# Performance work log

Measured on AMD Instinct MI355X. Metric: run time of the kernel, lower is better.

Reference implementation:

```python
import jax, jax.numpy as jnp
import numpy as np

B, N, K, F_IN, F_OUT = 2, 196608, 9, 64, 64


def setup_inputs() -> dict:
    key = jax.random.key(0)
    k1, k2, k3 = jax.random.split(key, 3)
    x = jax.random.normal(k1, (B, N, F_IN), dtype=jnp.float32)
    adjc = jax.random.randint(k2, (N, K), 0, N, dtype=jnp.int64)
    # first neighbor is the cell itself (typical grid adjacency)
    adjc = adjc.at[:, 0].set(jnp.arange(N, dtype=jnp.int64))
    scale = 1.0 / np.sqrt(K * F_IN)
    W = jax.random.normal(k3, (K, F_IN, F_OUT), dtype=jnp.float32) * scale
    b = jnp.zeros((F_OUT,), dtype=jnp.float32)
    return {"x": x, "adjc": adjc, "W": W, "b": b}


def reference(x, adjc, W, b):
    # get_nh: irregular gather of neighbor features -> [B, N, K, F_in]
    x_nh = x[:, adjc, :]
    # learned layer: contract over (neighborhood, in_features) -> [B, N, F_out]
    out = jnp.einsum("bnkf,kfo->bno", x_nh, W) + b
    return out
```

## Files before the change

### kernel.cpp

```cpp
#include <hip/hip_runtime.h>

#define B_ 2
#define N_ 196608
#define K_ 9
#define F_ 64
#define ROWS 64
#define ROWB 256

typedef __attribute__((ext_vector_type(8))) short short8;
typedef __attribute__((ext_vector_type(4))) unsigned short ushort4v;
typedef __attribute__((ext_vector_type(4))) float f32x4;

__device__ __forceinline__ unsigned short f2bf(float f) {
  unsigned u = __builtin_bit_cast(unsigned, f);
  u = (u + 0x7fffu + ((u >> 16) & 1u)) >> 16;
  return (unsigned short)u;
}

__global__ __launch_bounds__(256) void cvt_x_kernel(const float* __restrict__ x,
                                                    unsigned short* __restrict__ xb) {
  const int b = blockIdx.y;
  const long cidx = (long)blockIdx.x * 256 + threadIdx.x;
  const long n = cidx >> 4;
  const int qd = (int)(cidx & 15);
  const float4 v = *(const float4*)(x + ((size_t)b * N_ + n) * F_ + (size_t)qd * 4);
  ushort4v r;
  r[0] = f2bf(v.x); r[1] = f2bf(v.y); r[2] = f2bf(v.z); r[3] = f2bf(v.w);
  *(ushort4v*)(xb + ((size_t)n * 2 + b) * F_ + qd * 4) = r;
}

__global__ __launch_bounds__(256) void cvt_w_kernel(const float* __restrict__ W,
                                                    unsigned short* __restrict__ wt) {
  const int i = blockIdx.x * 256 + threadIdx.x;
  const int k = i >> 12;
  const int rem = i & 4095;
  const int o = rem >> 6;
  const int f = rem & 63;
  wt[i] = f2bf(W[(k << 12) + (f << 6) + o]);
}

__global__ __launch_bounds__(64, 1) void nhconv_main(
    const short* __restrict__ xb,
    const int* __restrict__ adjc,
    const short* __restrict__ wt,
    const float* __restrict__ bias,
    float* __restrict__ out) {
  __shared__ short abuf[3][ROWS * 128];
  __shared__ int s_adj[ROWS * K_];

  const int l = (int)threadIdx.x;
  const int n0 = blockIdx.x * ROWS;
  const int q = l >> 4;
  const int c = l & 15;

  for (int i = l; i < ROWS * K_; i += 64)
    s_adj[i] = __builtin_nontemporal_load(adjc + (size_t)n0 * K_ + i);

  auto stage = [&](int k, int bf) {
#pragma unroll
    for (int j = 0; j < 16; ++j) {
      const int row = j * 4 + (l >> 4);
      const int src_chunk = (l & 15) ^ (row & 7);
      const size_t goff = (size_t)(unsigned)s_adj[row * K_ + k] * ROWB + (src_chunk << 4);
      const char* src = (const char*)xb + goff;
      short* dst = &abuf[bf][(j * 4) * 128];
      __builtin_amdgcn_global_load_lds(
          (const __attribute__((address_space(1))) unsigned int*)src,
          (__attribute__((address_space(3))) unsigned int*)dst, 16, 0, 0);
    }
  };

  const short* wbase = wt + q * 8 + (c << 6);
  short8 rw[2][8];
  auto wload = [&](int k, int par) {
#pragma unroll
    for (int fs = 0; fs < 2; ++fs)
#pragma unroll
      for (int ct = 0; ct < 4; ++ct)
        rw[par][fs * 4 + ct] = *(const short8*)(wbase + (k << 12) + fs * 32 + (ct << 10));
  };

  f32x4 acc[2][4][4];
#pragma unroll
  for (int p = 0; p < 2; ++p)
#pragma unroll
    for (int rt = 0; rt < 4; ++rt)
#pragma unroll
      for (int ct = 0; ct < 4; ++ct)
        acc[p][rt][ct] = (f32x4){0.f, 0.f, 0.f, 0.f};

  wload(0, 0);
  stage(0, 0);
  wload(1, 1);
  stage(1, 1);

#pragma unroll
  for (int k = 0; k < K_; ++k) {
    asm volatile("s_waitcnt lgkmcnt(0)" ::: "memory");
    if (k >= 1 && k + 1 < K_) wload(k + 1, (k + 1) & 1);
    if (k + 2 < K_) stage(k + 2, (k + 2) % 3);

    if (k <= K_ - 3) {
      asm volatile("s_waitcnt vmcnt(40)" ::: "memory");
    } else if (k == K_ - 2) {
      asm volatile("s_waitcnt vmcnt(24)" ::: "memory");
    } else {
      asm volatile("s_waitcnt vmcnt(0)" ::: "memory");
    }
    __builtin_amdgcn_sched_barrier(0);

    const short* bufk = abuf[k % 3];
#pragma unroll
    for (int fs = 0; fs < 2; ++fs) {
#pragma unroll
      for (int rt = 0; rt < 4; ++rt) {
        const int arow = (rt * 16 + c) * 128;
        const int ch0 = (fs * 4 + q) ^ (c & 7);
        const int ch1 = (8 + fs * 4 + q) ^ (c & 7);
        const short8 a0 = *(const short8*)&bufk[arow + (ch0 << 3)];
        const short8 a1 = *(const short8*)&bufk[arow + (ch1 << 3)];
#pragma unroll
        for (int ct = 0; ct < 4; ++ct) {
          const short8 bfr = rw[k & 1][fs * 4 + ct];
          acc[0][rt][ct] =
              __builtin_amdgcn_mfma_f32_16x16x32_bf16(a0, bfr, acc[0][rt][ct], 0, 0, 0);
          acc[1][rt][ct] =
              __builtin_amdgcn_mfma_f32_16x16x32_bf16(a1, bfr, acc[1][rt][ct], 0, 0, 0);
        }
      }
    }
  }

  float bv[4];
#pragma unroll
  for (int ct = 0; ct < 4; ++ct) bv[ct] = bias[ct * 16 + c];

#pragma unroll
  for (int p = 0; p < 2; ++p) {
    const size_t outbase = ((size_t)p * N_ + (size_t)n0) * F_;
#pragma unroll
    for (int rt = 0; rt < 4; ++rt) {
#pragma unroll
      for (int ct = 0; ct < 4; ++ct) {
#pragma unroll
        for (int rr = 0; rr < 4; ++rr) {
          const int row = rt * 16 + q * 4 + rr;
          __builtin_nontemporal_store(acc[p][rt][ct][rr] + bv[ct],
                                      &out[outbase + (size_t)row * F_ + ct * 16 + c]);
        }
      }
    }
  }
}

extern "C" void kernel_launch(void* const* d_in, const int* in_sizes, int n_in,
                              void* d_out, int out_size, void* d_ws, size_t ws_size,
                              hipStream_t stream) {
  const float* x = (const float*)d_in[0];
  const int* adjc = (const int*)d_in[1];
  const float* W = (const float*)d_in[2];
  const float* bias = (const float*)d_in[3];
  float* out = (float*)d_out;

  unsigned short* xb = (unsigned short*)d_ws;
  unsigned short* wt = (unsigned short*)((char*)d_ws + (size_t)B_ * N_ * F_ * 2);

  cvt_x_kernel<<<dim3(N_ * 16 / 256, B_), 256, 0, stream>>>(x, xb);
  cvt_w_kernel<<<144, 256, 0, stream>>>(W, wt);

  nhconv_main<<<N_ / ROWS, 64, 0, stream>>>((const short*)xb, adjc, (const short*)wt,
                                            bias, out);
}
```

Measured before the change: 263.5 us.

## Load gathered neighbor rows directly into registers and merge conversion kernels

The main kernel stops staging gathered neighbor rows through LDS with global_load_lds and a triple buffer. Each lane now loads its A fragments straight from global memory into registers, double-buffered across the neighborhood loop. Adjacency indices are held per lane in registers, and the rows per workgroup drop from 64 to 32 with launch bounds raised to two blocks per SIMD. The x and W bf16 conversion kernels are merged into one launch. This removes LDS traffic and explicit waitcnt scheduling in exchange for more register pressure, smaller tiles, and possibly less coalesced 16-byte gathers.

```diff
diff --git a/kernel.cpp b/kernel.cpp
--- a/kernel.cpp
+++ b/kernel.cpp
@@ -4,8 +4,7 @@
 #define N_ 196608
 #define K_ 9
 #define F_ 64
-#define ROWS 64
-#define ROWB 256
+#define WROWS 32
 
 typedef __attribute__((ext_vector_type(8))) short short8;
 typedef __attribute__((ext_vector_type(4))) unsigned short ushort4v;
@@ -17,61 +16,65 @@
   return (unsigned short)u;
 }
 
-__global__ __launch_bounds__(256) void cvt_x_kernel(const float* __restrict__ x,
-                                                    unsigned short* __restrict__ xb) {
-  const int b = blockIdx.y;
-  const long cidx = (long)blockIdx.x * 256 + threadIdx.x;
-  const long n = cidx >> 4;
-  const int qd = (int)(cidx & 15);
-  const float4 v = *(const float4*)(x + ((size_t)b * N_ + n) * F_ + (size_t)qd * 4);
-  ushort4v r;
-  r[0] = f2bf(v.x); r[1] = f2bf(v.y); r[2] = f2bf(v.z); r[3] = f2bf(v.w);
-  *(ushort4v*)(xb + ((size_t)n * 2 + b) * F_ + qd * 4) = r;
+#define XCHUNKS (2L * N_ * 16)
+#define XBLK ((int)(XCHUNKS / 256))
+__global__ __launch_bounds__(256) void cvt_kernel(const float* __restrict__ x,
+                                                  unsigned short* __restrict__ xb,
+                                                  const float* __restrict__ W,
+                                                  unsigned short* __restrict__ wt) {
+  if (blockIdx.x < (unsigned)XBLK) {
+    const long i = (long)blockIdx.x * 256 + threadIdx.x;
+    const long pn = (long)N_ * 16;
+    const int b = (int)(i >= pn);
+    const long ci = i - (long)b * pn;
+    const long n = ci >> 4;
+    const int qd = (int)(ci & 15);
+    const float4 v = *(const float4*)(x + ((size_t)b * N_ + n) * F_ + (size_t)qd * 4);
+    ushort4v r;
+    r[0] = f2bf(v.x); r[1] = f2bf(v.y); r[2] = f2bf(v.z); r[3] = f2bf(v.w);
+    *(ushort4v*)(xb + ((size_t)n * 2 + b) * F_ + qd * 4) = r;
+  } else {
+    const int i = (blockIdx.x - XBLK) * 256 + threadIdx.x;
+    const int k = i >> 12;
+    const int rem = i & 4095;
+    const int o = rem >> 6;
+    const int f = rem & 63;
+    wt[i] = f2bf(W[(k << 12) + (f << 6) + o]);
+  }
 }
 
-__global__ __launch_bounds__(256) void cvt_w_kernel(const float* __restrict__ W,
-                                                    unsigned short* __restrict__ wt) {
-  const int i = blockIdx.x * 256 + threadIdx.x;
-  const int k = i >> 12;
-  const int rem = i & 4095;
-  const int o = rem >> 6;
-  const int f = rem & 63;
-  wt[i] = f2bf(W[(k << 12) + (f << 6) + o]);
-}
-
-__global__ __launch_bounds__(64, 1) void nhconv_main(
+__global__ __launch_bounds__(64, 2) void nhconv_main(
     const short* __restrict__ xb,
     const int* __restrict__ adjc,
     const short* __restrict__ wt,
     const float* __restrict__ bias,
     float* __restrict__ out) {
-  __shared__ short abuf[3][ROWS * 128];
-  __shared__ int s_adj[ROWS * K_];
-
   const int l = (int)threadIdx.x;
-  const int n0 = blockIdx.x * ROWS;
+  const int n0 = blockIdx.x * WROWS;
   const int q = l >> 4;
   const int c = l & 15;
 
-  for (int i = l; i < ROWS * K_; i += 64)
-    s_adj[i] = __builtin_nontemporal_load(adjc + (size_t)n0 * K_ + i);
+  int aj[2][K_];
+#pragma unroll
+  for (int rt = 0; rt < 2; ++rt) {
+    const int* ap = adjc + (size_t)(n0 + rt * 16 + c) * K_;
+#pragma unroll
+    for (int k = 0; k < K_; ++k) aj[rt][k] = ap[k];
+  }
 
-  auto stage = [&](int k, int bf) {
+  short8 ra[2][8], rw[2][8];
+  const short* wbase = wt + q * 8 + (c << 6);
+
+  auto aload = [&](int k, int par) {
 #pragma unroll
-    for (int j = 0; j < 16; ++j) {
-      const int row = j * 4 + (l >> 4);
-      const int src_chunk = (l & 15) ^ (row & 7);
-      const size_t goff = (size_t)(unsigned)s_adj[row * K_ + k] * ROWB + (src_chunk << 4);
-      const char* src = (const char*)xb + goff;
-      short* dst = &abuf[bf][(j * 4) * 128];
-      __builtin_amdgcn_global_load_lds(
-          (const __attribute__((address_space(1))) unsigned int*)src,
-          (__attribute__((address_space(3))) unsigned int*)dst, 16, 0, 0);
-    }
+    for (int p = 0; p < 2; ++p)
+#pragma unroll
+      for (int fs = 0; fs < 2; ++fs)
+#pragma unroll
+        for (int rt = 0; rt < 2; ++rt)
+          ra[par][p * 4 + fs * 2 + rt] = *(const short8*)(
+              xb + ((size_t)(unsigned)aj[rt][k] << 7) + p * 64 + fs * 32 + q * 8);
   };
-
-  const short* wbase = wt + q * 8 + (c << 6);
-  short8 rw[2][8];
   auto wload = [&](int k, int par) {
 #pragma unroll
     for (int fs = 0; fs < 2; ++fs)
@@ -80,55 +83,36 @@
         rw[par][fs * 4 + ct] = *(const short8*)(wbase + (k << 12) + fs * 32 + (ct << 10));
   };
 
-  f32x4 acc[2][4][4];
+  f32x4 acc[2][2][4];
 #pragma unroll
   for (int p = 0; p < 2; ++p)
 #pragma unroll
-    for (int rt = 0; rt < 4; ++rt)
+    for (int rt = 0; rt < 2; ++rt)
 #pragma unroll
       for (int ct = 0; ct < 4; ++ct)
         acc[p][rt][ct] = (f32x4){0.f, 0.f, 0.f, 0.f};
 
+  aload(0, 0);
   wload(0, 0);
-  stage(0, 0);
-  wload(1, 1);
-  stage(1, 1);
 
 #pragma unroll
   for (int k = 0; k < K_; ++k) {
-    asm volatile("s_waitcnt lgkmcnt(0)" ::: "memory");
-    if (k >= 1 && k + 1 < K_) wload(k + 1, (k + 1) & 1);
-    if (k + 2 < K_) stage(k + 2, (k + 2) % 3);
-
-    if (k <= K_ - 3) {
-      asm volatile("s_waitcnt vmcnt(40)" ::: "memory");
-    } else if (k == K_ - 2) {
-      asm volatile("s_waitcnt vmcnt(24)" ::: "memory");
-    } else {
-      asm volatile("s_waitcnt vmcnt(0)" ::: "memory");
+    if (k + 1 < K_) {
+      aload(k + 1, (k + 1) & 1);
+      wload(k + 1, (k + 1) & 1);
     }
-    __builtin_amdgcn_sched_barrier(0);
-
-    const short* bufk = abuf[k % 3];
 #pragma unroll
-    for (int fs = 0; fs < 2; ++fs) {
+    for (int fs = 0; fs < 2; ++fs)
 #pragma unroll
-      for (int rt = 0; rt < 4; ++rt) {
-        const int arow = (rt * 16 + c) * 128;
-        const int ch0 = (fs * 4 + q) ^ (c & 7);
-        const int ch1 = (8 + fs * 4 + q) ^ (c & 7);
-        const short8 a0 = *(const short8*)&bufk[arow + (ch0 << 3)];
-        const short8 a1 = *(const short8*)&bufk[arow + (ch1 << 3)];
+      for (int rt = 0; rt < 2; ++rt)
 #pragma unroll
         for (int ct = 0; ct < 4; ++ct) {
           const short8 bfr = rw[k & 1][fs * 4 + ct];
-          acc[0][rt][ct] =
-              __builtin_amdgcn_mfma_f32_16x16x32_bf16(a0, bfr, acc[0][rt][ct], 0, 0, 0);
-          acc[1][rt][ct] =
-              __builtin_amdgcn_mfma_f32_16x16x32_bf16(a1, bfr, acc[1][rt][ct], 0, 0, 0);
+          acc[0][rt][ct] = __builtin_amdgcn_mfma_f32_16x16x32_bf16(
+              ra[k & 1][0 + fs * 2 + rt], bfr, acc[0][rt][ct], 0, 0, 0);
+          acc[1][rt][ct] = __builtin_amdgcn_mfma_f32_16x16x32_bf16(
+              ra[k & 1][4 + fs * 2 + rt], bfr, acc[1][rt][ct], 0, 0, 0);
         }
-      }
-    }
   }
 
   float bv[4];
@@ -139,7 +123,7 @@
   for (int p = 0; p < 2; ++p) {
     const size_t outbase = ((size_t)p * N_ + (size_t)n0) * F_;
 #pragma unroll
-    for (int rt = 0; rt < 4; ++rt) {
+    for (int rt = 0; rt < 2; ++rt) {
 #pragma unroll
       for (int ct = 0; ct < 4; ++ct) {
 #pragma unroll
@@ -165,9 +149,8 @@
   unsigned short* xb = (unsigned short*)d_ws;
   unsigned short* wt = (unsigned short*)((char*)d_ws + (size_t)B_ * N_ * F_ * 2);
 
-  cvt_x_kernel<<<dim3(N_ * 16 / 256, B_), 256, 0, stream>>>(x, xb);
-  cvt_w_kernel<<<144, 256, 0, stream>>>(W, wt);
+  cvt_kernel<<<XBLK + 144, 256, 0, stream>>>(x, xb, W, wt);
 
-  nhconv_main<<<N_ / ROWS, 64, 0, stream>>>((const short*)xb, adjc, (const short*)wt,
-                                            bias, out);
+  nhconv_main<<<N_ / WROWS, 64, 0, stream>>>((const short*)xb, adjc, (const short*)wt,
+                                             bias, out);
 }
```

Result: slower. 288.5 us (+9.5%).
